# Performance work log

Measured on AMD Instinct MI355X. Metric: run time of the kernel, lower is better.

## Reference

```python
import jax, jax.numpy as jnp
import numpy as np

GRID_SIZE = 5
SPLINE_ORDER = 3
B, D, O = 16384, 512, 512


def _make_grid():
    h = 2.0 / GRID_SIZE
    # matches torch.arange(-k, grid_size + k + 1) * h - 2.0  -> 12 knots
    return jnp.arange(-SPLINE_ORDER, GRID_SIZE + SPLINE_ORDER + 1, dtype=jnp.float32) * h - 2.0


def _bspline_basis(x, grid):
    # x: [B, D]; grid: [G] with G = grid_size + 2*order + 1 = 12
    G = grid.shape[0]
    xe = x[..., None]                      # [B, D, 1]
    g = grid.reshape(1, 1, G)              # [1, 1, G]
    # degree-0: indicator of knot interval  -> [B, D, G-1]
    bases = ((xe >= g[:, :, :-1]) & (xe < g[:, :, 1:])).astype(x.dtype)
    eps = 1e-9
    for k in range(1, SPLINE_ORDER + 1):   # Cox-de Boor recursion, width shrinks by 1 each step
        left = (xe - g[:, :, :-k - 1]) / (g[:, :, k:-1] - g[:, :, :-k - 1] + eps)
        right = (g[:, :, k + 1:] - xe) / (g[:, :, k + 1:] - g[:, :, 1:-k] + eps)
        bases = left * bases[..., :-1] + right * bases[..., 1:]
    return bases                           # [B, D, grid_size + order] = [B, D, 8]


def setup_inputs() -> dict:
    key = jax.random.key(0)
    k1, k2, k3 = jax.random.split(key, 3)
    x = jax.random.normal(k1, (B, D), dtype=jnp.float32)
    # kaiming_uniform_(a=sqrt(5)*0.1): bound = sqrt(6 / ((1 + a^2) * fan_in))
    a = np.sqrt(5.0) * 0.1
    bound = float(np.sqrt(6.0 / ((1.0 + a * a) * D)))
    base_weight = jax.random.uniform(k2, (O, D), dtype=jnp.float32, minval=-bound, maxval=bound)
    spline_weight = jax.random.normal(k3, (O, D, GRID_SIZE + SPLINE_ORDER), dtype=jnp.float32) * 0.01
    return {"x": x, "base_weight": base_weight, "spline_weight": spline_weight}


def reference(x, base_weight, spline_weight):
    grid = _make_grid()
    base_output = jnp.matmul(jax.nn.silu(x), base_weight.T)      # [B, O]
    x_norm = jnp.clip(x, -2.0, 2.0)
    basis = _bspline_basis(x_norm, grid)                          # [B, D, 8]
    spline_output = jnp.einsum('bic,oic->bo', basis, spline_weight)
    return base_output + spline_output
```

## Files before the change

### kernel.cpp

```cpp
#include <hip/hip_runtime.h>
#include <cstdint>
#include <cstddef>
#include <type_traits>

#define B_ROWS 16384
#define D_DIM  512
#define O_DIM  512
#define K_DIM  4608
#define BM 64
#define BN 256
#define BK 32

typedef __bf16 bf16;
typedef __attribute__((ext_vector_type(8))) bf16  bf16x8;
typedef __attribute__((ext_vector_type(4))) float f32x4;

__device__ __forceinline__ void async_load16(const void* g, void* l) {
    __builtin_amdgcn_global_load_lds(
        (const __attribute__((address_space(1))) void*)g,
        (__attribute__((address_space(3))) void*)l,
        16, 0, 0);
}

__device__ __forceinline__ uint32_t pk2(float a, float b) {
    uint16_t ua = __builtin_bit_cast(uint16_t, (__bf16)a);
    uint16_t ub = __builtin_bit_cast(uint16_t, (__bf16)b);
    return (uint32_t)ua | ((uint32_t)ub << 16);
}

__device__ __forceinline__ void spline_pairs(float xv, uint32_t out[4]) {
    float xn = fminf(fmaxf(xv, -2.0f), 2.0f);
    float t  = (xn + 3.2f) * 2.5f;
    int   j0 = (int)t;
    float u  = t - (float)j0;
    float u2 = u * u, u3 = u2 * u, omu = 1.0f - u;
    const float s6 = 1.0f / 6.0f;
    float w0 = omu * omu * omu * s6;
    float w1 = (3.0f * u3 - 6.0f * u2 + 4.0f) * s6;
    float w2 = (-3.0f * u3 + 3.0f * u2 + 3.0f * u + 1.0f) * s6;
    float w3 = u3 * s6;
    uint64_t W64 = ((uint64_t)pk2(w2, w3) << 32) | pk2(w0, w1);
    int sh = (j0 - 3) * 16;
    uint64_t lo = W64 << (sh & 63);
    uint64_t hi = W64 >> ((64 - sh) & 63);
    uint32_t lo_lo = (uint32_t)lo, lo_hi = (uint32_t)(lo >> 32);
    uint32_t hi_lo = (uint32_t)hi, hi_hi = (uint32_t)(hi >> 32);
    bool lt64 = sh < 64, eq0 = (sh == 0), lt128 = sh < 128;
    out[0] = lt64 ? lo_lo : 0u;
    out[1] = lt64 ? lo_hi : 0u;
    out[2] = lt64 ? (eq0 ? 0u : hi_lo) : (lt128 ? lo_lo : 0u);
    out[3] = lt64 ? (eq0 ? 0u : hi_hi) : (lt128 ? lo_hi : 0u);
}

__global__ void pack_w_kernel(const float* __restrict__ bw,
                              const float* __restrict__ sw,
                              bf16* __restrict__ W) {
    int idx = blockIdx.x * blockDim.x + threadIdx.x;
    if (idx >= O_DIM * 64) return;
    int o  = idx >> 6;
    int i0 = (idx & 63) * 8;

    bf16 ob[9][8];
    const float* bwp = bw + (size_t)o * D_DIM + i0;
#pragma unroll
    for (int e = 0; e < 8; e++) {
        ob[0][e] = (bf16)bwp[e];
        const float* sp = sw + ((size_t)o * D_DIM + i0 + e) * 8;
#pragma unroll
        for (int c = 0; c < 8; c++)
            ob[c + 1][e] = (bf16)sp[c];
    }
    bf16* row = W + (size_t)o * K_DIM + i0;
#pragma unroll
    for (int f = 0; f < 9; f++)
        *(bf16x8*)(row + (size_t)f * D_DIM) = *(const bf16x8*)ob[f];
}

__global__ __launch_bounds__(256, 2)
void gemm_fused_kernel(const float* __restrict__ x, const bf16* __restrict__ W,
                       float* __restrict__ C) {
    __shared__ __align__(16) bf16 As[2][BM * BK];
    __shared__ __align__(16) bf16 Bs[2][BN * BK];

    const int tid  = threadIdx.x;
    const int n0   = blockIdx.x * BN;
    const int m0   = blockIdx.y * BM;
    const int wave = tid >> 6;
    const int lane = tid & 63;
    const int wn   = wave * 64;
    const int l15  = lane & 15;
    const int quad = lane >> 4;

    const int rA = tid >> 2;
    const int q8 = tid & 3;
    const float* xrow = x + (size_t)(m0 + rA) * D_DIM + q8 * 8;
    const int aslot = q8 ^ ((rA >> 1) & 3);
    bf16* aw0 = &As[0][rA * BK + aslot * 8];
    bf16* aw1 = &As[1][rA * BK + aslot * 8];

    const int sr = tid >> 2;
    const int sc = ((tid & 3) ^ ((sr >> 1) & 3)) * 8;
    const bf16* gB = W + (size_t)(n0 + sr) * K_DIM + sc;
    bf16* lb0 = &Bs[0][tid * 8];
    bf16* lb1 = &Bs[1][tid * 8];

    const int swz  = (l15 >> 1) & 3;
    const int aoff = l15 * BK + (quad ^ swz) * 8;
    const int boff = (wn + l15) * BK + (quad ^ swz) * 8;

    f32x4 acc[4][4] = {};
    uint32_t vpk[2][4][8];
    float xe[8];

    {
        float4 a = *(const float4*)xrow;
        float4 b = *(const float4*)(xrow + 4);
        xe[0]=a.x; xe[1]=a.y; xe[2]=a.z; xe[3]=a.w;
        xe[4]=b.x; xe[5]=b.y; xe[6]=b.z; xe[7]=b.w;
#pragma unroll
        for (int e = 0; e < 8; e++) {
            uint32_t o4[4];
            spline_pairs(xe[e], o4);
            vpk[0][0][e]=o4[0]; vpk[0][1][e]=o4[1];
            vpk[0][2][e]=o4[2]; vpk[0][3][e]=o4[3];
        }
        float sl[8];
#pragma unroll
        for (int e = 0; e < 8; e++)
            sl[e] = xe[e] * __builtin_amdgcn_rcpf(1.0f + __expf(-xe[e]));
        uint32_t o[4] = {pk2(sl[0],sl[1]), pk2(sl[2],sl[3]),
                         pk2(sl[4],sl[5]), pk2(sl[6],sl[7])};
        *(uint4*)aw0 = *(const uint4*)o;
#pragma unroll
        for (int j = 0; j < 4; j++)
            async_load16(gB + (size_t)j * 64 * K_DIM, lb0 + j * 2048);
    }
    __syncthreads();

    auto chunk_body = [&](auto pcv, int c) {
        constexpr int PC = decltype(pcv)::value;
#pragma unroll
        for (int f = 0; f < 9; f++) {
            const bf16* Asr = As[(PC + f) & 1];
            const bf16* Bsr = Bs[(PC + f) & 1];
            bf16* lbn = ((PC + f) & 1) ? lb0 : lb1;
            bf16* awn = ((PC + f) & 1) ? aw0 : aw1;
            const bool haveNext = !(c == 15 && f == 8);

            if (haveNext) {
                int koff = (f < 8) ? ((f + 1) * D_DIM + c * 32) : ((c + 1) * 32);
#pragma unroll
                for (int j = 0; j < 4; j++)
                    async_load16(gB + (size_t)j * 64 * K_DIM + koff, lbn + j * 2048);
            }
            if (f == 0 && c < 15) {
                float4 a = *(const float4*)(xrow + (c + 1) * 32);
                float4 b = *(const float4*)(xrow + (c + 1) * 32 + 4);
                xe[0]=a.x; xe[1]=a.y; xe[2]=a.z; xe[3]=a.w;
                xe[4]=b.x; xe[5]=b.y; xe[6]=b.z; xe[7]=b.w;
            }
            if (f >= 1 && c < 15) {
                uint32_t o4[4];
                spline_pairs(xe[f - 1], o4);
                vpk[PC ^ 1][0][f-1]=o4[0]; vpk[PC ^ 1][1][f-1]=o4[1];
                vpk[PC ^ 1][2][f-1]=o4[2]; vpk[PC ^ 1][3][f-1]=o4[3];
            }
            if (haveNext) {
                uint32_t o[4];
                if (f < 8) {
                    const int pr = f >> 1;
#pragma unroll
                    for (int m = 0; m < 4; m++) {
                        uint32_t lo = vpk[PC][pr][2*m], hi = vpk[PC][pr][2*m+1];
                        o[m] = (f & 1) ? ((lo >> 16) | (hi & 0xFFFF0000u))
                                       : ((lo & 0xFFFFu) | (hi << 16));
                    }
                } else {
                    float sl[8];
#pragma unroll
                    for (int e = 0; e < 8; e++)
                        sl[e] = xe[e] * __builtin_amdgcn_rcpf(1.0f + __expf(-xe[e]));
                    o[0]=pk2(sl[0],sl[1]); o[1]=pk2(sl[2],sl[3]);
                    o[2]=pk2(sl[4],sl[5]); o[3]=pk2(sl[6],sl[7]);
                }
                *(uint4*)awn = *(const uint4*)o;
            }

            bf16x8 af[4], bfr[4];
#pragma unroll
            for (int tt = 0; tt < 4; tt++)
                af[tt] = *(const bf16x8*)(Asr + aoff + tt * 16 * BK);
#pragma unroll
            for (int tt = 0; tt < 4; tt++)
                bfr[tt] = *(const bf16x8*)(Bsr + boff + tt * 16 * BK);
#pragma unroll
            for (int im = 0; im < 4; im++)
#pragma unroll
                for (int jn = 0; jn < 4; jn++)
                    acc[im][jn] = __builtin_amdgcn_mfma_f32_16x16x32_bf16(
                        af[im], bfr[jn], acc[im][jn], 0, 0, 0);
            __syncthreads();
        }
    };

    for (int cc = 0; cc < 16; cc += 2) {
        chunk_body(std::integral_constant<int,0>{}, cc);
        chunk_body(std::integral_constant<int,1>{}, cc + 1);
    }

#pragma unroll
    for (int im = 0; im < 4; im++) {
        const int rbase = m0 + im * 16 + quad * 4;
#pragma unroll
        for (int jn = 0; jn < 4; jn++) {
            const int col = n0 + wn + jn * 16 + l15;
#pragma unroll
            for (int rr = 0; rr < 4; rr++)
                C[(size_t)(rbase + rr) * O_DIM + col] = acc[im][jn][rr];
        }
    }
}

extern "C" void kernel_launch(void* const* d_in, const int* in_sizes, int n_in,
                              void* d_out, int out_size, void* d_ws, size_t ws_size,
                              hipStream_t stream) {
    const float* x  = (const float*)d_in[0];
    const float* bw = (const float*)d_in[1];
    const float* sw = (const float*)d_in[2];
    float* out = (float*)d_out;

    const size_t Wbytes = (size_t)O_DIM * K_DIM * sizeof(bf16);
    if (ws_size < Wbytes) return;
    bf16* W = (bf16*)d_ws;

    pack_w_kernel<<<(O_DIM * 64 + 255) / 256, 256, 0, stream>>>(bw, sw, W);
    gemm_fused_kernel<<<dim3(O_DIM / BN, B_ROWS / BM), 256, 0, stream>>>(x, W, out);
}
```

Before: 191.0 us.

## Use 512-thread blocks with 8 waves each covering 32 output columns

Doubles the threads per block from 256 to 512. Each wave now computes a 64x32 tile instead of 64x64, and the A-tile spline/SiLU production and B-tile async loads are split across twice as many threads. The goal is more latency hiding and more parallel spline basis computation per block, at the cost of fewer MFMAs per LDS fragment load. A fragments are also now read redundantly by twice as many waves.

```diff
diff --git a/kernel.cpp b/kernel.cpp
--- a/kernel.cpp
+++ b/kernel.cpp
@@ -76,7 +76,7 @@
         *(bf16x8*)(row + (size_t)f * D_DIM) = *(const bf16x8*)ob[f];
 }
 
-__global__ __launch_bounds__(256, 2)
+__global__ __launch_bounds__(512, 4)
 void gemm_fused_kernel(const float* __restrict__ x, const bf16* __restrict__ W,
                        float* __restrict__ C) {
     __shared__ __align__(16) bf16 As[2][BM * BK];
@@ -87,16 +87,17 @@
     const int m0   = blockIdx.y * BM;
     const int wave = tid >> 6;
     const int lane = tid & 63;
-    const int wn   = wave * 64;
+    const int wn   = wave * 32;
     const int l15  = lane & 15;
     const int quad = lane >> 4;
 
-    const int rA = tid >> 2;
-    const int q8 = tid & 3;
-    const float* xrow = x + (size_t)(m0 + rA) * D_DIM + q8 * 8;
-    const int aslot = q8 ^ ((rA >> 1) & 3);
-    bf16* aw0 = &As[0][rA * BK + aslot * 8];
-    bf16* aw1 = &As[1][rA * BK + aslot * 8];
+    const int rA = tid >> 3;
+    const int q8 = tid & 7;
+    const float* xrow = x + (size_t)(m0 + rA) * D_DIM + q8 * 4;
+    const int ps = (q8 >> 1) ^ ((rA >> 1) & 3);
+    const int hh = q8 & 1;
+    bf16* aw0 = &As[0][rA * BK + ps * 8 + hh * 4];
+    bf16* aw1 = &As[1][rA * BK + ps * 8 + hh * 4];
 
     const int sr = tid >> 2;
     const int sc = ((tid & 3) ^ ((sr >> 1) & 3)) * 8;
@@ -108,32 +109,28 @@
     const int aoff = l15 * BK + (quad ^ swz) * 8;
     const int boff = (wn + l15) * BK + (quad ^ swz) * 8;
 
-    f32x4 acc[4][4] = {};
-    uint32_t vpk[2][4][8];
-    float xe[8];
+    f32x4 acc[4][2] = {};
+    uint32_t vpk[2][4][4];
+    float xe[4];
 
     {
         float4 a = *(const float4*)xrow;
-        float4 b = *(const float4*)(xrow + 4);
         xe[0]=a.x; xe[1]=a.y; xe[2]=a.z; xe[3]=a.w;
-        xe[4]=b.x; xe[5]=b.y; xe[6]=b.z; xe[7]=b.w;
-#pragma unroll
-        for (int e = 0; e < 8; e++) {
+#pragma unroll
+        for (int e = 0; e < 4; e++) {
             uint32_t o4[4];
             spline_pairs(xe[e], o4);
             vpk[0][0][e]=o4[0]; vpk[0][1][e]=o4[1];
             vpk[0][2][e]=o4[2]; vpk[0][3][e]=o4[3];
         }
-        float sl[8];
-#pragma unroll
-        for (int e = 0; e < 8; e++)
+        float sl[4];
+#pragma unroll
+        for (int e = 0; e < 4; e++)
             sl[e] = xe[e] * __builtin_amdgcn_rcpf(1.0f + __expf(-xe[e]));
-        uint32_t o[4] = {pk2(sl[0],sl[1]), pk2(sl[2],sl[3]),
-                         pk2(sl[4],sl[5]), pk2(sl[6],sl[7])};
-        *(uint4*)aw0 = *(const uint4*)o;
-#pragma unroll
-        for (int j = 0; j < 4; j++)
-            async_load16(gB + (size_t)j * 64 * K_DIM, lb0 + j * 2048);
+        uint32_t o[2] = {pk2(sl[0],sl[1]), pk2(sl[2],sl[3])};
+        *(uint2*)aw0 = *(const uint2*)o;
+        async_load16(gB, lb0);
+        async_load16(gB + (size_t)128 * K_DIM, lb0 + 4096);
     }
     __syncthreads();
 
@@ -141,62 +138,59 @@
         constexpr int PC = decltype(pcv)::value;
 #pragma unroll
         for (int f = 0; f < 9; f++) {
-            const bf16* Asr = As[(PC + f) & 1];
-            const bf16* Bsr = Bs[(PC + f) & 1];
-            bf16* lbn = ((PC + f) & 1) ? lb0 : lb1;
-            bf16* awn = ((PC + f) & 1) ? aw0 : aw1;
+            const int cur = (PC + f) & 1;
+            const bf16* Asr = As[cur];
+            const bf16* Bsr = Bs[cur];
+            bf16* lbn = cur ? lb0 : lb1;
+            bf16* awn = cur ? aw0 : aw1;
             const bool haveNext = !(c == 15 && f == 8);
 
             if (haveNext) {
                 int koff = (f < 8) ? ((f + 1) * D_DIM + c * 32) : ((c + 1) * 32);
-#pragma unroll
-                for (int j = 0; j < 4; j++)
-                    async_load16(gB + (size_t)j * 64 * K_DIM + koff, lbn + j * 2048);
+                async_load16(gB + koff, lbn);
+                async_load16(gB + (size_t)128 * K_DIM + koff, lbn + 4096);
             }
             if (f == 0 && c < 15) {
                 float4 a = *(const float4*)(xrow + (c + 1) * 32);
-                float4 b = *(const float4*)(xrow + (c + 1) * 32 + 4);
                 xe[0]=a.x; xe[1]=a.y; xe[2]=a.z; xe[3]=a.w;
-                xe[4]=b.x; xe[5]=b.y; xe[6]=b.z; xe[7]=b.w;
-            }
-            if (f >= 1 && c < 15) {
+            }
+            if (f >= 1 && f <= 4 && c < 15) {
                 uint32_t o4[4];
                 spline_pairs(xe[f - 1], o4);
                 vpk[PC ^ 1][0][f-1]=o4[0]; vpk[PC ^ 1][1][f-1]=o4[1];
                 vpk[PC ^ 1][2][f-1]=o4[2]; vpk[PC ^ 1][3][f-1]=o4[3];
             }
             if (haveNext) {
-                uint32_t o[4];
+                uint32_t o[2];
                 if (f < 8) {
                     const int pr = f >> 1;
 #pragma unroll
-                    for (int m = 0; m < 4; m++) {
+                    for (int m = 0; m < 2; m++) {
                         uint32_t lo = vpk[PC][pr][2*m], hi = vpk[PC][pr][2*m+1];
                         o[m] = (f & 1) ? ((lo >> 16) | (hi & 0xFFFF0000u))
                                        : ((lo & 0xFFFFu) | (hi << 16));
                     }
                 } else {
-                    float sl[8];
-#pragma unroll
-                    for (int e = 0; e < 8; e++)
+                    float sl[4];
+#pragma unroll
+                    for (int e = 0; e < 4; e++)
                         sl[e] = xe[e] * __builtin_amdgcn_rcpf(1.0f + __expf(-xe[e]));
-                    o[0]=pk2(sl[0],sl[1]); o[1]=pk2(sl[2],sl[3]);
-                    o[2]=pk2(sl[4],sl[5]); o[3]=pk2(sl[6],sl[7]);
+                    o[0] = pk2(sl[0],sl[1]); o[1] = pk2(sl[2],sl[3]);
                 }
-                *(uint4*)awn = *(const uint4*)o;
-            }
-
-            bf16x8 af[4], bfr[4];
+                *(uint2*)awn = *(const uint2*)o;
+            }
+
+            bf16x8 af[4], bfr[2];
 #pragma unroll
             for (int tt = 0; tt < 4; tt++)
                 af[tt] = *(const bf16x8*)(Asr + aoff + tt * 16 * BK);
 #pragma unroll
-            for (int tt = 0; tt < 4; tt++)
-                bfr[tt] = *(const bf16x8*)(Bsr + boff + tt * 16 * BK);
+            for (int jn = 0; jn < 2; jn++)
+                bfr[jn] = *(const bf16x8*)(Bsr + boff + jn * 16 * BK);
 #pragma unroll
             for (int im = 0; im < 4; im++)
 #pragma unroll
-                for (int jn = 0; jn < 4; jn++)
+                for (int jn = 0; jn < 2; jn++)
                     acc[im][jn] = __builtin_amdgcn_mfma_f32_16x16x32_bf16(
                         af[im], bfr[jn], acc[im][jn], 0, 0, 0);
             __syncthreads();
@@ -212,7 +206,7 @@
     for (int im = 0; im < 4; im++) {
         const int rbase = m0 + im * 16 + quad * 4;
 #pragma unroll
-        for (int jn = 0; jn < 4; jn++) {
+        for (int jn = 0; jn < 2; jn++) {
             const int col = n0 + wn + jn * 16 + l15;
 #pragma unroll
             for (int rr = 0; rr < 4; rr++)
@@ -234,5 +228,5 @@
     bf16* W = (bf16*)d_ws;
 
     pack_w_kernel<<<(O_DIM * 64 + 255) / 256, 256, 0, stream>>>(bw, sw, W);
-    gemm_fused_kernel<<<dim3(O_DIM / BN, B_ROWS / BM), 256, 0, stream>>>(x, W, out);
-}
+    gemm_fused_kernel<<<dim3(O_DIM / BN, B_ROWS / BM), 512, 0, stream>>>(x, W, out);
+}
```

Result: no change. 187.6 us (-1.7%).
